# Kernel tuning notes

Hardware: AMD Instinct MI355X
Metric: run time of the kernel (lower is better)

Reference implementation:

```python
import jax, jax.numpy as jnp
import numpy as np

D_MODEL = 1024
SCALE = 1.0 / np.sqrt(D_MODEL).astype(np.float32)


def setup_inputs() -> dict:
    key = jax.random.key(0)
    ks = jax.random.split(key, 9)
    B, S, D = 4, 2048, D_MODEL
    init = 1.0 / np.sqrt(D).astype(np.float32)
    return {
        "q": jax.random.normal(ks[0], (B, S, D), jnp.float32),
        "k": jax.random.normal(ks[1], (B, S, D), jnp.float32),
        "v": jax.random.normal(ks[2], (B, S, D), jnp.float32),
        "Wq": jax.random.uniform(ks[3], (D, D), jnp.float32, -init, init),
        "bq": jax.random.uniform(ks[4], (D,), jnp.float32, -init, init),
        "Wk": jax.random.uniform(ks[5], (D, D), jnp.float32, -init, init),
        "bk": jax.random.uniform(ks[6], (D,), jnp.float32, -init, init),
        "Wv": jax.random.uniform(ks[7], (D, D), jnp.float32, -init, init),
        "bv": jax.random.uniform(ks[8], (D,), jnp.float32, -init, init),
    }


def reference(q, k, v, Wq, bq, Wk, bk, Wv, bv):
    # Linear projections (torch Linear: x @ W.T + b)
    qp = jnp.einsum('bsd,ed->bse', q, Wq) + bq
    kp = jnp.einsum('bsd,ed->bse', k, Wk) + bk
    vp = jnp.einsum('bsd,ed->bse', v, Wv) + bv
    qp = jax.nn.softmax(qp, axis=-1)          # softmax over feature dim
    kp = jax.nn.softmax(kp, axis=-2) * SCALE  # softmax over sequence dim
    vp = jax.nn.softmax(vp, axis=-2)          # softmax over sequence dim
    attn_weights = jnp.einsum('bqd,bkd->bqk', qp, kp)  # [B,S,S]
    output = jnp.einsum('bqk,bkd->bqd', attn_weights, vp)
    return (output, attn_weights)
```

## Files before the change

kernel.cpp:

```cpp
#include <hip/hip_runtime.h>
#include <math.h>


typedef float  f32x4  __attribute__((ext_vector_type(4)));
typedef __bf16 bf16x8 __attribute__((ext_vector_type(8)));
typedef int    i32x4  __attribute__((ext_vector_type(4)));
typedef unsigned short u16;

__device__ __forceinline__ float b2f(u16 u) {
    unsigned int i = ((unsigned int)u) << 16; float f;
    __builtin_memcpy(&f, &i, 4); return f;
}
__device__ __forceinline__ u16 f2b(float f) {
    unsigned int i; __builtin_memcpy(&i, &f, 4);
    i += 0x7FFFu + ((i >> 16) & 1u);
    return (u16)(i >> 16);
}

__global__ __launch_bounds__(256) void cvt_all(
    const float4* __restrict__ q, const float4* __restrict__ k,
    const float4* __restrict__ v, const float4* __restrict__ Wq,
    const float4* __restrict__ Wk, const float4* __restrict__ Wv,
    const float* __restrict__ bq, const float* __restrict__ bk,
    const float* __restrict__ bv,
    ushort4* __restrict__ qb, ushort4* __restrict__ kb,
    ushort4* __restrict__ vb, ushort4* __restrict__ Wb,
    float* __restrict__ biasCat)
{
    int bid = blockIdx.x, t = threadIdx.x;
    const float4* s; ushort4* d; int idx;
    if (bid < 8192)       { s = q;  d = qb;            idx = bid * 256 + t; }
    else if (bid < 16384) { s = k;  d = kb;            idx = (bid - 8192) * 256 + t; }
    else if (bid < 24576) { s = v;  d = vb;            idx = (bid - 16384) * 256 + t; }
    else if (bid < 25600) { s = Wq; d = Wb;            idx = (bid - 24576) * 256 + t; }
    else if (bid < 26624) { s = Wk; d = Wb + 262144;   idx = (bid - 25600) * 256 + t; }
    else if (bid < 27648) { s = Wv; d = Wb + 524288;   idx = (bid - 26624) * 256 + t; }
    else {
        for (int i = t; i < 3072; i += 256)
            biasCat[i] = (i < 1024) ? bq[i] : (i < 2048) ? bk[i - 1024] : bv[i - 2048];
        return;
    }
    float4 vv = s[idx];
    ushort4 o;
    o.x = f2b(vv.x); o.y = f2b(vv.y); o.z = f2b(vv.z); o.w = f2b(vv.w);
    d[idx] = o;
}

template<int EPI, int BN>
__global__ __launch_bounds__(512, 2) void gemm256(
    const u16* __restrict__ Ap, const u16* __restrict__ Bp,
    float* __restrict__ C32, u16* __restrict__ C16, u16* __restrict__ Calt,
    const float* __restrict__ bias,
    int N, int K, long long sA, long long sB, long long sC)
{
    constexpr int NB2 = BN / 128;
    constexpr int BH  = BN * 32;
    constexpr int LDSN = 32768 + 4 * BH;
    __shared__ __align__(16) u16 lds[LDSN];

    const int tid  = threadIdx.x;
    const int lane = tid & 63;
    const int w    = tid >> 6;
    const int wr   = w >> 2, wc = w & 3;

    const int gx  = gridDim.x;
    const int tot = gx * gridDim.y;
    const int lin = blockIdx.y * gx + blockIdx.x;
    const int vlin = (lin & 7) * (tot >> 3) + (lin >> 3);
    const int bx = vlin % gx, by = vlin / gx;
    const int m0 = by * 256, n0 = bx * BN;
    const int z  = blockIdx.z;

    const u16* Ag = Ap + (size_t)z * sA;
    const u16* Bg = Bp + (size_t)z * sB;

    const int cl = tid ^ ((tid & 32) >> 4);
    const int lr = cl >> 3;
    const int ce = (cl & 7) * 8;
    const int arow = m0 + lr;
    const int brow = (BN == 256) ? (n0 + (lr & 31) + ((lr & 32) << 1))
                                 : (n0 + lr);

    const int axr = ((lane >> 2) & 1) << 4;
    const int ar0 = (wr * 64 + (lane & 15)) * 64 + (lane >> 4) * 8;
    const int br0 = (BN == 256)
        ? ((wc * 32 + (lane & 15)) * 64 + (lane >> 4) * 8)
        : ((wc * 16 + (lane & 15)) * 64 + (lane >> 4) * 8);

#define GLL16(gsrc, ldsoff)                                                    \
    __builtin_amdgcn_global_load_lds(                                          \
        (__attribute__((address_space(1))) void*)(uintptr_t)(gsrc),            \
        (__attribute__((address_space(3))) void*)&lds[ldsoff], 16, 0, 0)

#define STAGE_A(c, h, T)                                                       \
    do { const u16* _s = Ag + (size_t)(arow + (h) * 64) * K + (T) * 64 + ce;   \
         int _d = (((c) << 1) + (h)) * 8192 + tid * 8;                         \
         GLL16(_s, _d); GLL16(_s + (size_t)128 * K, _d + 4096); } while (0)

#define STAGE_B(c, g, T)                                                       \
    do { if constexpr (BN == 256) {                                            \
             const u16* _s = Bg + (size_t)(brow + (g) * 32) * K + (T) * 64 + ce; \
             int _d = 32768 + (((c) << 1) + (g)) * 8192 + tid * 8;             \
             GLL16(_s, _d); GLL16(_s + (size_t)128 * K, _d + 4096);            \
         } else {                                                              \
             const u16* _s = Bg + (size_t)(brow + (g) * 64) * K + (T) * 64 + ce; \
             int _d = 32768 + (((c) << 1) + (g)) * 4096 + tid * 8;             \
             GLL16(_s, _d);                                                    \
         } } while (0)

#define SBAR asm volatile("s_barrier" ::: "memory")
#define LGKM0 do { asm volatile("s_waitcnt lgkmcnt(0)" ::: "memory");          \
                   __builtin_amdgcn_sched_barrier(0); } while (0)
#define VMBOUND do { if constexpr (BN == 256)                                  \
                         asm volatile("s_waitcnt vmcnt(4)" ::: "memory");      \
                     else asm volatile("s_waitcnt vmcnt(3)" ::: "memory"); } while (0)

#define LDA(base)                                                              \
    _Pragma("unroll") for (int mi2 = 0; mi2 < 4; ++mi2)                        \
    _Pragma("unroll") for (int ks = 0; ks < 2; ++ks)                           \
        afr[mi2][ks] = __builtin_bit_cast(bf16x8,                              \
            *(const i32x4*)&lds[(base) + ((ar0 + mi2 * 1024 + ks * 32) ^ axr)]);

#define LDB(dst, base)                                                         \
    _Pragma("unroll") for (int ni2 = 0; ni2 < NB2; ++ni2)                      \
    _Pragma("unroll") for (int ks = 0; ks < 2; ++ks)                           \
        dst[ni2][ks] = __builtin_bit_cast(bf16x8,                              \
            *(const i32x4*)&lds[(base) + ((br0 + ni2 * 1024 + ks * 32) ^ axr)]);

#define MFMA_Q(mb, nb, bfrag)                                                  \
    __builtin_amdgcn_s_setprio(1);                                             \
    _Pragma("unroll") for (int mi2 = 0; mi2 < 4; ++mi2)                        \
    _Pragma("unroll") for (int ni2 = 0; ni2 < NB2; ++ni2)                      \
    _Pragma("unroll") for (int ks = 0; ks < 2; ++ks)                           \
        acc[(mb) + mi2][(nb) + ni2] = __builtin_amdgcn_mfma_f32_16x16x32_bf16( \
            afr[mi2][ks], bfrag[ni2][ks], acc[(mb) + mi2][(nb) + ni2], 0, 0, 0); \
    __builtin_amdgcn_s_setprio(0)

    f32x4 acc[8][2 * NB2];
#pragma unroll
    for (int i = 0; i < 8; ++i)
#pragma unroll
        for (int j = 0; j < 2 * NB2; ++j) acc[i][j] = (f32x4)0.0f;

    bf16x8 afr[4][2], b0f[NB2][2], b1f[NB2][2];

    const int nt = K >> 6;

    STAGE_A(0, 0, 0); STAGE_B(0, 0, 0);
    STAGE_A(0, 1, 0); STAGE_B(0, 1, 0);
    STAGE_A(1, 0, 1); STAGE_B(1, 0, 1);

    for (int T = 0; T < nt; ++T) {
        const int cur = T & 1, nxt = cur ^ 1;
        const int ab = (cur << 1) * 8192;
        const int bb = 32768 + (cur << 1) * BH;

        if (T + 1 < nt) VMBOUND;
        else            asm volatile("s_waitcnt vmcnt(0)" ::: "memory");
        SBAR;
        LDA(ab); LDB(b0f, bb);
        if (T + 1 < nt) STAGE_B(nxt, 1, T + 1);
        SBAR; LGKM0;
        MFMA_Q(0, 0, b0f);
        SBAR;
        LDB(b1f, bb + BH);
        if (T + 1 < nt) STAGE_A(nxt, 1, T + 1);
        SBAR; LGKM0;
        MFMA_Q(0, NB2, b1f);
        SBAR;
        LDA(ab + 8192);
        if (T + 2 < nt) STAGE_A(cur, 0, T + 2);
        SBAR; LGKM0;
        MFMA_Q(4, 0, b0f);
        SBAR;
        if (T + 2 < nt) STAGE_B(cur, 0, T + 2);
        SBAR; LGKM0;
        MFMA_Q(4, NB2, b1f);
        SBAR;
    }

    const int cr0 = m0 + wr * 128 + ((lane >> 4) << 2);

    if constexpr (EPI == 0) {
        const int cc0 = n0 + wc * 64 + (lane & 15);
        float* Cg = C32 + (size_t)z * sC;
#pragma unroll
        for (int mi = 0; mi < 8; ++mi)
#pragma unroll
            for (int ni = 0; ni < 4; ++ni)
#pragma unroll
                for (int j = 0; j < 4; ++j)
                    Cg[(size_t)(cr0 + mi * 16 + j) * N + cc0 + ni * 16] = acc[mi][ni][j];

        u16* sE = lds;
        u16* Cb = C16 + (size_t)z * sC;
        const int wrow0 = ((lane >> 4) << 2);
        const int wcol0 = wc * 64 + (lane & 15);
        const int rr = tid >> 2;
        const int c0 = (tid & 3) * 8;
        __syncthreads();
#pragma unroll
        for (int p = 0; p < 2; ++p) {
            if (wr == p) {
#pragma unroll
                for (int mi = 0; mi < 8; ++mi)
#pragma unroll
                    for (int ni = 0; ni < 4; ++ni)
#pragma unroll
                        for (int j = 0; j < 4; ++j)
                            sE[(wrow0 + mi * 16 + j) * 264 + wcol0 + ni * 16] =
                                f2b(acc[mi][ni][j]);
            }
            __syncthreads();
#pragma unroll
            for (int i = 0; i < 8; ++i) {
                i32x4 vv = *(const i32x4*)&sE[rr * 264 + c0 + i * 32];
                *(i32x4*)&Cb[(size_t)(m0 + p * 128 + rr) * N + n0 + c0 + i * 32] = vv;
            }
            if (p == 0) __syncthreads();
        }
    } else if constexpr (EPI == 1) {
        u16* sE = lds;
        u16* Cb = (z == 2) ? Calt : (C16 + (size_t)z * sC);
        const int colb = wc * 16 + (lane & 15);
        const float bv0 = bias[(size_t)z * 1024 + n0 + colb];
        const float bv1 = bias[(size_t)z * 1024 + n0 + 64 + colb];
        const int wrow0 = ((lane >> 4) << 2);
        const int rr = tid >> 2, t4 = tid & 3;
        __syncthreads();
#pragma unroll
        for (int p = 0; p < 2; ++p) {
            if (wr == p) {
#pragma unroll
                for (int mi = 0; mi < 8; ++mi)
#pragma unroll
                    for (int j = 0; j < 4; ++j) {
                        int row = wrow0 + mi * 16 + j;
                        sE[row * 136 + colb]      = f2b(__expf(acc[mi][0][j] + bv0));
                        sE[row * 136 + 64 + colb] = f2b(__expf(acc[mi][1][j] + bv1));
                    }
            }
            __syncthreads();
#pragma unroll
            for (int i = 0; i < 4; ++i) {
                i32x4 vv = *(const i32x4*)&sE[rr * 136 + (t4 + i * 4) * 8];
                *(i32x4*)&Cb[(size_t)(m0 + p * 128 + rr) * N + n0 + (t4 + i * 4) * 8] = vv;
            }
            if (p == 0) __syncthreads();
        }
    } else {
        float* Cg = C32 + (size_t)z * sC;
        const int colb = wc * 16 + (lane & 15);
#pragma unroll
        for (int mi = 0; mi < 8; ++mi)
#pragma unroll
            for (int ni = 0; ni < 2; ++ni)
#pragma unroll
                for (int j = 0; j < 4; ++j)
                    Cg[(size_t)(cr0 + mi * 16 + j) * N + n0 + ni * 64 + colb] =
                        acc[mi][ni][j];
    }
#undef GLL16
#undef STAGE_A
#undef STAGE_B
#undef SBAR
#undef LGKM0
#undef VMBOUND
#undef LDA
#undef LDB
#undef MFMA_Q
}

__global__ __launch_bounds__(256) void sm_partials(
    u16* __restrict__ qE, const u16* __restrict__ kE, const u16* __restrict__ vE,
    float* __restrict__ kpart, float* __restrict__ vpart)
{
    int bid = blockIdx.x, t = threadIdx.x;
    if (bid < 8192) {
        u16* p = qE + (size_t)bid * 1024;
        ushort4 v = *(ushort4*)&p[t * 4];
        float e0 = b2f(v.x), e1 = b2f(v.y), e2 = b2f(v.z), e3 = b2f(v.w);
        float s = (e0 + e1) + (e2 + e3);
#pragma unroll
        for (int off = 32; off; off >>= 1) s += __shfl_down(s, off);
        __shared__ float red[4];
        if ((t & 63) == 0) red[t >> 6] = s;
        __syncthreads();
        float inv = 1.0f / ((red[0] + red[1]) + (red[2] + red[3]));
        ushort4 o;
        o.x = f2b(e0 * inv); o.y = f2b(e1 * inv);
        o.z = f2b(e2 * inv); o.w = f2b(e3 * inv);
        *(ushort4*)&p[t * 4] = o;
    } else {
        int j = bid - 8192;
        const u16* d; float* part;
        if (j < 64) { d = kE; part = kpart; } else { d = vE; part = vpart; j -= 64; }
        int b = j >> 4, c = j & 15;
        const u16* base = d + ((size_t)b * 2048 + c * 128) * 1024 + t * 4;
        float a0 = 0, a1 = 0, a2 = 0, a3 = 0;
        for (int s = 0; s < 128; ++s) {
            ushort4 v = *(const ushort4*)(base + (size_t)s * 1024);
            a0 += b2f(v.x); a1 += b2f(v.y); a2 += b2f(v.z); a3 += b2f(v.w);
        }
        *(float4*)(part + ((size_t)(b * 16 + c)) * 1024 + t * 4) = make_float4(a0, a1, a2, a3);
    }
}

__global__ __launch_bounds__(256) void col_reduce2(
    const float* __restrict__ kpart, const float* __restrict__ vpart,
    float* __restrict__ kinv, float* __restrict__ vinv)
{
    int bid = blockIdx.x;
    const float* part; float* inv; float mult;
    if (bid < 16) { part = kpart; inv = kinv; mult = 0.03125f; }
    else          { part = vpart; inv = vinv; mult = 1.0f; bid -= 16; }
    int idx = bid * 256 + threadIdx.x;
    int b = idx >> 10, e = idx & 1023;
    float s = 0;
    for (int c = 0; c < 16; ++c) s += part[((size_t)(b * 16 + c)) * 1024 + e];
    inv[idx] = mult / s;
}

__global__ __launch_bounds__(256) void norm_all(
    u16* __restrict__ kE, const float* __restrict__ kinv,
    const u16* __restrict__ vE, const float* __restrict__ vinv,
    u16* __restrict__ vpT)
{
    int bid = blockIdx.x, t = threadIdx.x;
    if (bid < 8192) {
        int b = bid >> 11, s = bid & 2047;
        u16* p = kE + ((size_t)b * 2048 + s) * 1024 + t * 4;
        float4 iv = *(const float4*)(kinv + b * 1024 + t * 4);
        ushort4 v = *(ushort4*)p;
        v.x = f2b(b2f(v.x) * iv.x); v.y = f2b(b2f(v.y) * iv.y);
        v.z = f2b(b2f(v.z) * iv.z); v.w = f2b(b2f(v.w) * iv.w);
        *(ushort4*)p = v;
    } else {
        __shared__ __align__(16) u16 tile[64][68];
        int j = bid - 8192;
        int b = j >> 9, y = (j >> 5) & 15, x = j & 31;
        int s0 = x * 64, e0 = y * 64;
        int lr = t >> 4, lc = (t & 15) * 4;
#pragma unroll
        for (int i = 0; i < 4; ++i) {
            int sr = i * 16 + lr;
            ushort4 v = *(const ushort4*)(vE + ((size_t)b * 2048 + s0 + sr) * 1024 + e0 + lc);
            tile[sr][lc] = v.x; tile[sr][lc + 1] = v.y;
            tile[sr][lc + 2] = v.z; tile[sr][lc + 3] = v.w;
        }
        __syncthreads();
#pragma unroll
        for (int i = 0; i < 4; ++i) {
            int er = i * 16 + lr;
            float iv = vinv[b * 1024 + e0 + er];
            ushort4 v;
            v.x = f2b(b2f(tile[lc + 0][er]) * iv);
            v.y = f2b(b2f(tile[lc + 1][er]) * iv);
            v.z = f2b(b2f(tile[lc + 2][er]) * iv);
            v.w = f2b(b2f(tile[lc + 3][er]) * iv);
            *(ushort4*)(vpT + ((size_t)b * 1024 + e0 + er) * 2048 + s0 + lc) = v;
        }
    }
}

extern "C" void kernel_launch(void* const* d_in, const int* in_sizes, int n_in,
                              void* d_out, int out_size, void* d_ws, size_t ws_size,
                              hipStream_t stream)
{
    const float* q  = (const float*)d_in[0];
    const float* k  = (const float*)d_in[1];
    const float* v  = (const float*)d_in[2];
    const float* Wq = (const float*)d_in[3];
    const float* bq = (const float*)d_in[4];
    const float* Wk = (const float*)d_in[5];
    const float* bk = (const float*)d_in[6];
    const float* Wv = (const float*)d_in[7];
    const float* bv = (const float*)d_in[8];

    float* out  = (float*)d_out;
    float* attn = out + 8388608;

    u16* wsU = (u16*)d_ws;
    u16* qE   = wsU;
    u16* kE   = wsU + 8388608;
    u16* Wb   = wsU + 16777216;
    u16* qb   = wsU + 25165824;
    u16* kb   = wsU + 33554432;
    u16* vb   = wsU + 41943040;
    u16* vpT  = wsU + 25165824;
    u16* attnB = wsU + 33554432;
    u16* vE   = (u16*)attn;

    float* tail  = (float*)(wsU + 50331648);
    float* kpart = tail;
    float* vpart = tail + 65536;
    float* kinv  = tail + 131072;
    float* vinv  = tail + 135168;
    float* biasCat = tail + 139264;

    const long long SD = 2048LL * 1024, SS = 2048LL * 2048, DS = 1024LL * 2048;

    cvt_all<<<dim3(27649), dim3(256), 0, stream>>>(
        (const float4*)q, (const float4*)k, (const float4*)v,
        (const float4*)Wq, (const float4*)Wk, (const float4*)Wv,
        bq, bk, bv,
        (ushort4*)qb, (ushort4*)kb, (ushort4*)vb, (ushort4*)Wb, biasCat);

    gemm256<1, 128><<<dim3(8, 32, 3), dim3(512), 0, stream>>>(
        qb, Wb, nullptr, qE, vE, biasCat,
        1024, 1024, 8388608LL, 1048576LL, 8388608LL);

    sm_partials<<<dim3(8320), dim3(256), 0, stream>>>(qE, kE, vE, kpart, vpart);

    col_reduce2<<<dim3(32), dim3(256), 0, stream>>>(kpart, vpart, kinv, vinv);

    norm_all<<<dim3(10240), dim3(256), 0, stream>>>(kE, kinv, vE, vinv, vpT);

    gemm256<0, 256><<<dim3(8, 8, 4), dim3(512), 0, stream>>>(
        qE, kE, attn, attnB, nullptr, nullptr, 2048, 1024, SD, SD, SS);

    gemm256<2, 128><<<dim3(8, 8, 4), dim3(512), 0, stream>>>(
        attnB, vpT, out, nullptr, nullptr, nullptr, 1024, 2048, SS, DS, SD);
}
```

Measured before the change: 245.4 us.

## Restructure BN=128 GEMM pipeline to two barrier phases and swizzle epilogue LDS

For the BN=128 GEMM variant, the K loop is rebuilt into two phases per tile. Both B fragments are loaded at once and staging is regrouped, which cuts the number of s_barrier/lgkmcnt waits per iteration from eight to two, with retuned vmcnt thresholds. The BN=256 path is kept but inlined. Both epilogues now XOR-swizzle LDS column addresses by row to reduce bank conflicts when staging bf16 output. Fewer barriers per tile risk read/write hazards on the LDS buffers if the vmcnt accounting is off.

```diff
diff --git a/kernel.cpp b/kernel.cpp
--- a/kernel.cpp
+++ b/kernel.cpp
@@ -111,9 +111,6 @@
 #define SBAR asm volatile("s_barrier" ::: "memory")
 #define LGKM0 do { asm volatile("s_waitcnt lgkmcnt(0)" ::: "memory");          \
                    __builtin_amdgcn_sched_barrier(0); } while (0)
-#define VMBOUND do { if constexpr (BN == 256)                                  \
-                         asm volatile("s_waitcnt vmcnt(4)" ::: "memory");      \
-                     else asm volatile("s_waitcnt vmcnt(3)" ::: "memory"); } while (0)
 
 #define LDA(base)                                                              \
     _Pragma("unroll") for (int mi2 = 0; mi2 < 4; ++mi2)                        \
@@ -146,37 +143,66 @@
 
     const int nt = K >> 6;
 
-    STAGE_A(0, 0, 0); STAGE_B(0, 0, 0);
-    STAGE_A(0, 1, 0); STAGE_B(0, 1, 0);
-    STAGE_A(1, 0, 1); STAGE_B(1, 0, 1);
-
-    for (int T = 0; T < nt; ++T) {
-        const int cur = T & 1, nxt = cur ^ 1;
-        const int ab = (cur << 1) * 8192;
-        const int bb = 32768 + (cur << 1) * BH;
-
-        if (T + 1 < nt) VMBOUND;
-        else            asm volatile("s_waitcnt vmcnt(0)" ::: "memory");
-        SBAR;
-        LDA(ab); LDB(b0f, bb);
-        if (T + 1 < nt) STAGE_B(nxt, 1, T + 1);
-        SBAR; LGKM0;
-        MFMA_Q(0, 0, b0f);
-        SBAR;
-        LDB(b1f, bb + BH);
-        if (T + 1 < nt) STAGE_A(nxt, 1, T + 1);
-        SBAR; LGKM0;
-        MFMA_Q(0, NB2, b1f);
-        SBAR;
-        LDA(ab + 8192);
-        if (T + 2 < nt) STAGE_A(cur, 0, T + 2);
-        SBAR; LGKM0;
-        MFMA_Q(4, 0, b0f);
-        SBAR;
-        if (T + 2 < nt) STAGE_B(cur, 0, T + 2);
-        SBAR; LGKM0;
-        MFMA_Q(4, NB2, b1f);
-        SBAR;
+    if constexpr (BN == 256) {
+        STAGE_A(0, 0, 0); STAGE_B(0, 0, 0);
+        STAGE_A(0, 1, 0); STAGE_B(0, 1, 0);
+        STAGE_A(1, 0, 1); STAGE_B(1, 0, 1);
+
+        for (int T = 0; T < nt; ++T) {
+            const int cur = T & 1, nxt = cur ^ 1;
+            const int ab = (cur << 1) * 8192;
+            const int bb = 32768 + (cur << 1) * BH;
+
+            if (T + 1 < nt) asm volatile("s_waitcnt vmcnt(4)" ::: "memory");
+            else            asm volatile("s_waitcnt vmcnt(0)" ::: "memory");
+            SBAR;
+            LDA(ab); LDB(b0f, bb);
+            if (T + 1 < nt) STAGE_B(nxt, 1, T + 1);
+            SBAR; LGKM0;
+            MFMA_Q(0, 0, b0f);
+            SBAR;
+            LDB(b1f, bb + BH);
+            if (T + 1 < nt) STAGE_A(nxt, 1, T + 1);
+            SBAR; LGKM0;
+            MFMA_Q(0, NB2, b1f);
+            SBAR;
+            LDA(ab + 8192);
+            if (T + 2 < nt) STAGE_A(cur, 0, T + 2);
+            SBAR; LGKM0;
+            MFMA_Q(4, 0, b0f);
+            SBAR;
+            if (T + 2 < nt) STAGE_B(cur, 0, T + 2);
+            SBAR; LGKM0;
+            MFMA_Q(4, NB2, b1f);
+            SBAR;
+        }
+    } else {
+        STAGE_A(0, 0, 0); STAGE_B(0, 0, 0); STAGE_B(0, 1, 0);
+        STAGE_A(0, 1, 0);
+        STAGE_A(1, 0, 1); STAGE_B(1, 0, 1); STAGE_B(1, 1, 1);
+
+        for (int T = 0; T < nt; ++T) {
+            const int cur = T & 1, nxt = cur ^ 1;
+            const int ab = (cur << 1) * 8192;
+            const int bb = 32768 + (cur << 1) * BH;
+
+            if (T + 1 < nt) asm volatile("s_waitcnt vmcnt(6)" ::: "memory");
+            else            asm volatile("s_waitcnt vmcnt(2)" ::: "memory");
+            SBAR;
+            LDA(ab); LDB(b0f, bb); LDB(b1f, bb + BH);
+            if (T + 1 < nt) STAGE_A(nxt, 1, T + 1);
+            LGKM0;
+            MFMA_Q(0, 0, b0f); MFMA_Q(0, 1, b1f);
+
+            if (T + 1 < nt) asm volatile("s_waitcnt vmcnt(6)" ::: "memory");
+            else            asm volatile("s_waitcnt vmcnt(0)" ::: "memory");
+            SBAR;
+            LDA(ab + 8192);
+            if (T + 2 < nt) { STAGE_A(cur, 0, T + 2); STAGE_B(cur, 0, T + 2);
+                              STAGE_B(cur, 1, T + 2); }
+            LGKM0;
+            MFMA_Q(4, 0, b0f); MFMA_Q(4, 1, b1f);
+        }
     }
 
     const int cr0 = m0 + wr * 128 + ((lane >> 4) << 2);
@@ -198,6 +224,7 @@
         const int wcol0 = wc * 64 + (lane & 15);
         const int rr = tid >> 2;
         const int c0 = (tid & 3) * 8;
+        const int rxor = ((rr >> 2) & 3) << 4;
         __syncthreads();
 #pragma unroll
         for (int p = 0; p < 2; ++p) {
@@ -205,16 +232,19 @@
 #pragma unroll
                 for (int mi = 0; mi < 8; ++mi)
 #pragma unroll
-                    for (int ni = 0; ni < 4; ++ni)
-#pragma unroll
-                        for (int j = 0; j < 4; ++j)
-                            sE[(wrow0 + mi * 16 + j) * 264 + wcol0 + ni * 16] =
+                    for (int j = 0; j < 4; ++j) {
+                        int row = wrow0 + mi * 16 + j;
+                        int cx = ((row >> 2) & 3) << 4;
+#pragma unroll
+                        for (int ni = 0; ni < 4; ++ni)
+                            sE[row * 264 + ((wcol0 + ni * 16) ^ cx)] =
                                 f2b(acc[mi][ni][j]);
+                    }
             }
             __syncthreads();
 #pragma unroll
             for (int i = 0; i < 8; ++i) {
-                i32x4 vv = *(const i32x4*)&sE[rr * 264 + c0 + i * 32];
+                i32x4 vv = *(const i32x4*)&sE[rr * 264 + ((c0 + i * 32) ^ rxor)];
                 *(i32x4*)&Cb[(size_t)(m0 + p * 128 + rr) * N + n0 + c0 + i * 32] = vv;
             }
             if (p == 0) __syncthreads();
@@ -227,6 +257,7 @@
         const float bv1 = bias[(size_t)z * 1024 + n0 + 64 + colb];
         const int wrow0 = ((lane >> 4) << 2);
         const int rr = tid >> 2, t4 = tid & 3;
+        const int rxor = ((rr >> 2) & 3) << 4;
         __syncthreads();
 #pragma unroll
         for (int p = 0; p < 2; ++p) {
@@ -236,14 +267,15 @@
 #pragma unroll
                     for (int j = 0; j < 4; ++j) {
                         int row = wrow0 + mi * 16 + j;
-                        sE[row * 136 + colb]      = f2b(__expf(acc[mi][0][j] + bv0));
-                        sE[row * 136 + 64 + colb] = f2b(__expf(acc[mi][1][j] + bv1));
+                        int cx = ((row >> 2) & 3) << 4;
+                        sE[row * 136 + (colb ^ cx)]        = f2b(__expf(acc[mi][0][j] + bv0));
+                        sE[row * 136 + ((64 + colb) ^ cx)] = f2b(__expf(acc[mi][1][j] + bv1));
                     }
             }
             __syncthreads();
 #pragma unroll
             for (int i = 0; i < 4; ++i) {
-                i32x4 vv = *(const i32x4*)&sE[rr * 136 + (t4 + i * 4) * 8];
+                i32x4 vv = *(const i32x4*)&sE[rr * 136 + (((t4 + i * 4) * 8) ^ rxor)];
                 *(i32x4*)&Cb[(size_t)(m0 + p * 128 + rr) * N + n0 + (t4 + i * 4) * 8] = vv;
             }
             if (p == 0) __syncthreads();
@@ -265,7 +297,6 @@
 #undef STAGE_B
 #undef SBAR
 #undef LGKM0
-#undef VMBOUND
 #undef LDA
 #undef LDB
 #undef MFMA_Q
```

Result: faster. 224.0 us (-8.7%).

## Use 128x128 tile GEMM for projections and output, widen LDS swizzle for attn GEMM

Applied to the files above, without the earlier changes.

Adds a new 128x128-tile GEMM kernel with 4 blocks per CU and a simpler two-phase K pipeline. It is used for the QKV projection and the attn@V GEMM, which doubles or quadruples their grid sizes to improve occupancy and CU load balance. The 256x256 QK^T kernel becomes a specialised non-template kernel with a wider XOR swizzle meant to cut LDS bank conflicts. Smaller tiles mean less data reuse per block and more global traffic.

```diff
diff --git a/kernel.cpp b/kernel.cpp
--- a/kernel.cpp
+++ b/kernel.cpp
@@ -46,17 +46,12 @@
     d[idx] = o;
 }
 
-template<int EPI, int BN>
-__global__ __launch_bounds__(512, 2) void gemm256(
+__global__ __launch_bounds__(512, 2) void gemm256_attn(
     const u16* __restrict__ Ap, const u16* __restrict__ Bp,
-    float* __restrict__ C32, u16* __restrict__ C16, u16* __restrict__ Calt,
-    const float* __restrict__ bias,
+    float* __restrict__ C32, u16* __restrict__ C16,
     int N, int K, long long sA, long long sB, long long sC)
 {
-    constexpr int NB2 = BN / 128;
-    constexpr int BH  = BN * 32;
-    constexpr int LDSN = 32768 + 4 * BH;
-    __shared__ __align__(16) u16 lds[LDSN];
+    __shared__ __align__(16) u16 lds[65536];
 
     const int tid  = threadIdx.x;
     const int lane = tid & 63;
@@ -68,24 +63,21 @@
     const int lin = blockIdx.y * gx + blockIdx.x;
     const int vlin = (lin & 7) * (tot >> 3) + (lin >> 3);
     const int bx = vlin % gx, by = vlin / gx;
-    const int m0 = by * 256, n0 = bx * BN;
+    const int m0 = by * 256, n0 = bx * 256;
     const int z  = blockIdx.z;
 
     const u16* Ag = Ap + (size_t)z * sA;
     const u16* Bg = Bp + (size_t)z * sB;
 
-    const int cl = tid ^ ((tid & 32) >> 4);
+    const int cl = tid ^ ((tid >> 4) & 6);
     const int lr = cl >> 3;
     const int ce = (cl & 7) * 8;
     const int arow = m0 + lr;
-    const int brow = (BN == 256) ? (n0 + (lr & 31) + ((lr & 32) << 1))
-                                 : (n0 + lr);
-
-    const int axr = ((lane >> 2) & 1) << 4;
+    const int brow = n0 + (lr & 31) + ((lr & 32) << 1);
+
+    const int axr = ((lane >> 2) & 3) << 4;
     const int ar0 = (wr * 64 + (lane & 15)) * 64 + (lane >> 4) * 8;
-    const int br0 = (BN == 256)
-        ? ((wc * 32 + (lane & 15)) * 64 + (lane >> 4) * 8)
-        : ((wc * 16 + (lane & 15)) * 64 + (lane >> 4) * 8);
+    const int br0 = (wc * 32 + (lane & 15)) * 64 + (lane >> 4) * 8;
 
 #define GLL16(gsrc, ldsoff)                                                    \
     __builtin_amdgcn_global_load_lds(                                          \
@@ -98,22 +90,13 @@
          GLL16(_s, _d); GLL16(_s + (size_t)128 * K, _d + 4096); } while (0)
 
 #define STAGE_B(c, g, T)                                                       \
-    do { if constexpr (BN == 256) {                                            \
-             const u16* _s = Bg + (size_t)(brow + (g) * 32) * K + (T) * 64 + ce; \
-             int _d = 32768 + (((c) << 1) + (g)) * 8192 + tid * 8;             \
-             GLL16(_s, _d); GLL16(_s + (size_t)128 * K, _d + 4096);            \
-         } else {                                                              \
-             const u16* _s = Bg + (size_t)(brow + (g) * 64) * K + (T) * 64 + ce; \
-             int _d = 32768 + (((c) << 1) + (g)) * 4096 + tid * 8;             \
-             GLL16(_s, _d);                                                    \
-         } } while (0)
+    do { const u16* _s = Bg + (size_t)(brow + (g) * 32) * K + (T) * 64 + ce;   \
+         int _d = 32768 + (((c) << 1) + (g)) * 8192 + tid * 8;                 \
+         GLL16(_s, _d); GLL16(_s + (size_t)128 * K, _d + 4096); } while (0)
 
 #define SBAR asm volatile("s_barrier" ::: "memory")
 #define LGKM0 do { asm volatile("s_waitcnt lgkmcnt(0)" ::: "memory");          \
                    __builtin_amdgcn_sched_barrier(0); } while (0)
-#define VMBOUND do { if constexpr (BN == 256)                                  \
-                         asm volatile("s_waitcnt vmcnt(4)" ::: "memory");      \
-                     else asm volatile("s_waitcnt vmcnt(3)" ::: "memory"); } while (0)
 
 #define LDA(base)                                                              \
     _Pragma("unroll") for (int mi2 = 0; mi2 < 4; ++mi2)                        \
@@ -122,7 +105,7 @@
             *(const i32x4*)&lds[(base) + ((ar0 + mi2 * 1024 + ks * 32) ^ axr)]);
 
 #define LDB(dst, base)                                                         \
-    _Pragma("unroll") for (int ni2 = 0; ni2 < NB2; ++ni2)                      \
+    _Pragma("unroll") for (int ni2 = 0; ni2 < 2; ++ni2)                        \
     _Pragma("unroll") for (int ks = 0; ks < 2; ++ks)                           \
         dst[ni2][ks] = __builtin_bit_cast(bf16x8,                              \
             *(const i32x4*)&lds[(base) + ((br0 + ni2 * 1024 + ks * 32) ^ axr)]);
@@ -130,19 +113,19 @@
 #define MFMA_Q(mb, nb, bfrag)                                                  \
     __builtin_amdgcn_s_setprio(1);                                             \
     _Pragma("unroll") for (int mi2 = 0; mi2 < 4; ++mi2)                        \
-    _Pragma("unroll") for (int ni2 = 0; ni2 < NB2; ++ni2)                      \
+    _Pragma("unroll") for (int ni2 = 0; ni2 < 2; ++ni2)                        \
     _Pragma("unroll") for (int ks = 0; ks < 2; ++ks)                           \
         acc[(mb) + mi2][(nb) + ni2] = __builtin_amdgcn_mfma_f32_16x16x32_bf16( \
             afr[mi2][ks], bfrag[ni2][ks], acc[(mb) + mi2][(nb) + ni2], 0, 0, 0); \
     __builtin_amdgcn_s_setprio(0)
 
-    f32x4 acc[8][2 * NB2];
+    f32x4 acc[8][4];
 #pragma unroll
     for (int i = 0; i < 8; ++i)
 #pragma unroll
-        for (int j = 0; j < 2 * NB2; ++j) acc[i][j] = (f32x4)0.0f;
-
-    bf16x8 afr[4][2], b0f[NB2][2], b1f[NB2][2];
+        for (int j = 0; j < 4; ++j) acc[i][j] = (f32x4)0.0f;
+
+    bf16x8 afr[4][2], b0f[2][2], b1f[2][2];
 
     const int nt = K >> 6;
 
@@ -153,9 +136,9 @@
     for (int T = 0; T < nt; ++T) {
         const int cur = T & 1, nxt = cur ^ 1;
         const int ab = (cur << 1) * 8192;
-        const int bb = 32768 + (cur << 1) * BH;
-
-        if (T + 1 < nt) VMBOUND;
+        const int bb = 32768 + (cur << 1) * 8192;
+
+        if (T + 1 < nt) asm volatile("s_waitcnt vmcnt(4)" ::: "memory");
         else            asm volatile("s_waitcnt vmcnt(0)" ::: "memory");
         SBAR;
         LDA(ab); LDB(b0f, bb);
@@ -163,10 +146,10 @@
         SBAR; LGKM0;
         MFMA_Q(0, 0, b0f);
         SBAR;
-        LDB(b1f, bb + BH);
+        LDB(b1f, bb + 8192);
         if (T + 1 < nt) STAGE_A(nxt, 1, T + 1);
         SBAR; LGKM0;
-        MFMA_Q(0, NB2, b1f);
+        MFMA_Q(0, 2, b1f);
         SBAR;
         LDA(ab + 8192);
         if (T + 2 < nt) STAGE_A(cur, 0, T + 2);
@@ -175,100 +158,199 @@
         SBAR;
         if (T + 2 < nt) STAGE_B(cur, 0, T + 2);
         SBAR; LGKM0;
-        MFMA_Q(4, NB2, b1f);
+        MFMA_Q(4, 2, b1f);
         SBAR;
     }
 
     const int cr0 = m0 + wr * 128 + ((lane >> 4) << 2);
-
-    if constexpr (EPI == 0) {
-        const int cc0 = n0 + wc * 64 + (lane & 15);
-        float* Cg = C32 + (size_t)z * sC;
-#pragma unroll
-        for (int mi = 0; mi < 8; ++mi)
-#pragma unroll
-            for (int ni = 0; ni < 4; ++ni)
-#pragma unroll
-                for (int j = 0; j < 4; ++j)
-                    Cg[(size_t)(cr0 + mi * 16 + j) * N + cc0 + ni * 16] = acc[mi][ni][j];
-
-        u16* sE = lds;
-        u16* Cb = C16 + (size_t)z * sC;
-        const int wrow0 = ((lane >> 4) << 2);
-        const int wcol0 = wc * 64 + (lane & 15);
-        const int rr = tid >> 2;
-        const int c0 = (tid & 3) * 8;
+    const int cc0 = n0 + wc * 64 + (lane & 15);
+    float* Cg = C32 + (size_t)z * sC;
+#pragma unroll
+    for (int mi = 0; mi < 8; ++mi)
+#pragma unroll
+        for (int ni = 0; ni < 4; ++ni)
+#pragma unroll
+            for (int j = 0; j < 4; ++j)
+                Cg[(size_t)(cr0 + mi * 16 + j) * N + cc0 + ni * 16] = acc[mi][ni][j];
+
+    u16* sE = lds;
+    u16* Cb = C16 + (size_t)z * sC;
+    const int wrow0 = ((lane >> 4) << 2);
+    const int wcol0 = wc * 64 + (lane & 15);
+    const int rr = tid >> 2;
+    const int c0 = (tid & 3) * 8;
+    __syncthreads();
+#pragma unroll
+    for (int p = 0; p < 2; ++p) {
+        if (wr == p) {
+#pragma unroll
+            for (int mi = 0; mi < 8; ++mi)
+#pragma unroll
+                for (int ni = 0; ni < 4; ++ni)
+#pragma unroll
+                    for (int j = 0; j < 4; ++j)
+                        sE[(wrow0 + mi * 16 + j) * 264 + wcol0 + ni * 16] =
+                            f2b(acc[mi][ni][j]);
+        }
         __syncthreads();
 #pragma unroll
-        for (int p = 0; p < 2; ++p) {
-            if (wr == p) {
-#pragma unroll
-                for (int mi = 0; mi < 8; ++mi)
-#pragma unroll
-                    for (int ni = 0; ni < 4; ++ni)
-#pragma unroll
-                        for (int j = 0; j < 4; ++j)
-                            sE[(wrow0 + mi * 16 + j) * 264 + wcol0 + ni * 16] =
-                                f2b(acc[mi][ni][j]);
-            }
-            __syncthreads();
-#pragma unroll
-            for (int i = 0; i < 8; ++i) {
-                i32x4 vv = *(const i32x4*)&sE[rr * 264 + c0 + i * 32];
-                *(i32x4*)&Cb[(size_t)(m0 + p * 128 + rr) * N + n0 + c0 + i * 32] = vv;
-            }
-            if (p == 0) __syncthreads();
+        for (int i = 0; i < 8; ++i) {
+            i32x4 vv = *(const i32x4*)&sE[rr * 264 + c0 + i * 32];
+            *(i32x4*)&Cb[(size_t)(m0 + p * 128 + rr) * N + n0 + c0 + i * 32] = vv;
         }
-    } else if constexpr (EPI == 1) {
+        if (p == 0) __syncthreads();
+    }
+#undef GLL16
+#undef STAGE_A
+#undef STAGE_B
+#undef LDA
+#undef LDB
+#undef MFMA_Q
+}
+
+template<int EPI>
+__global__ __launch_bounds__(512, 4) void gemm128(
+    const u16* __restrict__ Ap, const u16* __restrict__ Bp,
+    float* __restrict__ C32, u16* __restrict__ C16, u16* __restrict__ Calt,
+    const float* __restrict__ bias,
+    int N, int K, long long sA, long long sB, long long sC)
+{
+    __shared__ __align__(16) u16 lds[32768];
+
+    const int tid  = threadIdx.x;
+    const int lane = tid & 63;
+    const int w    = tid >> 6;
+    const int wr   = w >> 2, wc = w & 3;
+
+    const int gx  = gridDim.x;
+    const int tot = gx * gridDim.y;
+    const int lin = blockIdx.y * gx + blockIdx.x;
+    const int vlin = (lin & 7) * (tot >> 3) + (lin >> 3);
+    const int bx = vlin % gx, by = vlin / gx;
+    const int m0 = by * 128, n0 = bx * 128;
+    const int z  = blockIdx.z;
+
+    const u16* Ag = Ap + (size_t)z * sA;
+    const u16* Bg = Bp + (size_t)z * sB;
+
+    const int cl = tid ^ ((tid >> 3) & 3);
+    const int lr = cl >> 2;
+    const int ce = (cl & 3) * 8;
+    const int arow = m0 + lr, brow = n0 + lr;
+
+    const int exr = ((lane >> 1) & 3) << 3;
+    const int ar0 = (wr * 64 + (lane & 15)) * 32 + (lane >> 4) * 8;
+    const int br0 = (wc * 32 + (lane & 15)) * 32 + (lane >> 4) * 8;
+
+#define GLL16(gsrc, ldsoff)                                                    \
+    __builtin_amdgcn_global_load_lds(                                          \
+        (__attribute__((address_space(1))) void*)(uintptr_t)(gsrc),            \
+        (__attribute__((address_space(3))) void*)&lds[ldsoff], 16, 0, 0)
+
+#define STAGE_A(c, h, T)                                                       \
+    GLL16(Ag + (size_t)arow * K + (T) * 64 + (h) * 32 + ce,                    \
+          (((c) << 1) + (h)) * 4096 + tid * 8)
+
+#define STAGE_B(c, h, T)                                                       \
+    GLL16(Bg + (size_t)brow * K + (T) * 64 + (h) * 32 + ce,                    \
+          16384 + (((c) << 1) + (h)) * 4096 + tid * 8)
+
+#define LGKM0 do { asm volatile("s_waitcnt lgkmcnt(0)" ::: "memory");          \
+                   __builtin_amdgcn_sched_barrier(0); } while (0)
+
+#define LDAB(base)                                                             \
+    _Pragma("unroll") for (int mi2 = 0; mi2 < 4; ++mi2)                        \
+        afr[mi2] = __builtin_bit_cast(bf16x8,                                  \
+            *(const i32x4*)&lds[(base) + ((ar0 + mi2 * 512) ^ exr)]);          \
+    _Pragma("unroll") for (int ni2 = 0; ni2 < 2; ++ni2)                        \
+        bfr[ni2] = __builtin_bit_cast(bf16x8,                                  \
+            *(const i32x4*)&lds[16384 + (base) + ((br0 + ni2 * 512) ^ exr)]);
+
+#define MFMA8                                                                  \
+    __builtin_amdgcn_s_setprio(1);                                             \
+    _Pragma("unroll") for (int mi2 = 0; mi2 < 4; ++mi2)                        \
+    _Pragma("unroll") for (int ni2 = 0; ni2 < 2; ++ni2)                        \
+        acc[mi2][ni2] = __builtin_amdgcn_mfma_f32_16x16x32_bf16(               \
+            afr[mi2], bfr[ni2], acc[mi2][ni2], 0, 0, 0);                       \
+    __builtin_amdgcn_s_setprio(0)
+
+    f32x4 acc[4][2];
+#pragma unroll
+    for (int i = 0; i < 4; ++i)
+#pragma unroll
+        for (int j = 0; j < 2; ++j) acc[i][j] = (f32x4)0.0f;
+
+    bf16x8 afr[4], bfr[2];
+
+    const int nt = K >> 6;
+
+    STAGE_A(0, 0, 0); STAGE_B(0, 0, 0);
+    STAGE_A(0, 1, 0); STAGE_B(0, 1, 0);
+    STAGE_A(1, 0, 1); STAGE_B(1, 0, 1);
+
+    for (int T = 0; T < nt; ++T) {
+        const int cur = T & 1, nxt = cur ^ 1;
+        const int ab = (cur << 1) * 4096;
+
+        if (T + 1 < nt) asm volatile("s_waitcnt vmcnt(4)" ::: "memory");
+        else            asm volatile("s_waitcnt vmcnt(2)" ::: "memory");
+        asm volatile("s_barrier" ::: "memory");
+        LDAB(ab);
+        if (T + 1 < nt) { STAGE_A(nxt, 1, T + 1); STAGE_B(nxt, 1, T + 1); }
+        LGKM0;
+        MFMA8;
+
+        if (T + 1 < nt) asm volatile("s_waitcnt vmcnt(4)" ::: "memory");
+        else            asm volatile("s_waitcnt vmcnt(0)" ::: "memory");
+        asm volatile("s_barrier" ::: "memory");
+        LDAB(ab + 4096);
+        if (T + 2 < nt) { STAGE_A(cur, 0, T + 2); STAGE_B(cur, 0, T + 2); }
+        LGKM0;
+        MFMA8;
+    }
+
+    if constexpr (EPI == 1) {
         u16* sE = lds;
         u16* Cb = (z == 2) ? Calt : (C16 + (size_t)z * sC);
-        const int colb = wc * 16 + (lane & 15);
-        const float bv0 = bias[(size_t)z * 1024 + n0 + colb];
-        const float bv1 = bias[(size_t)z * 1024 + n0 + 64 + colb];
-        const int wrow0 = ((lane >> 4) << 2);
-        const int rr = tid >> 2, t4 = tid & 3;
+        const int colb = wc * 32 + (lane & 15);
+        float bv0 = bias[(size_t)z * 1024 + n0 + colb];
+        float bv1 = bias[(size_t)z * 1024 + n0 + colb + 16];
+        const int wrow0 = wr * 64 + ((lane >> 4) << 2);
         __syncthreads();
 #pragma unroll
-        for (int p = 0; p < 2; ++p) {
-            if (wr == p) {
-#pragma unroll
-                for (int mi = 0; mi < 8; ++mi)
-#pragma unroll
-                    for (int j = 0; j < 4; ++j) {
-                        int row = wrow0 + mi * 16 + j;
-                        sE[row * 136 + colb]      = f2b(__expf(acc[mi][0][j] + bv0));
-                        sE[row * 136 + 64 + colb] = f2b(__expf(acc[mi][1][j] + bv1));
-                    }
+        for (int mi = 0; mi < 4; ++mi)
+#pragma unroll
+            for (int j = 0; j < 4; ++j) {
+                int row = wrow0 + mi * 16 + j;
+                sE[row * 136 + colb]      = f2b(__expf(acc[mi][0][j] + bv0));
+                sE[row * 136 + colb + 16] = f2b(__expf(acc[mi][1][j] + bv1));
             }
-            __syncthreads();
-#pragma unroll
-            for (int i = 0; i < 4; ++i) {
-                i32x4 vv = *(const i32x4*)&sE[rr * 136 + (t4 + i * 4) * 8];
-                *(i32x4*)&Cb[(size_t)(m0 + p * 128 + rr) * N + n0 + (t4 + i * 4) * 8] = vv;
-            }
-            if (p == 0) __syncthreads();
+        __syncthreads();
+        const int rr = tid >> 2, c0 = (tid & 3) * 8;
+#pragma unroll
+        for (int i = 0; i < 4; ++i) {
+            i32x4 vv = *(const i32x4*)&sE[rr * 136 + c0 + i * 32];
+            *(i32x4*)&Cb[(size_t)(m0 + rr) * N + n0 + c0 + i * 32] = vv;
         }
     } else {
         float* Cg = C32 + (size_t)z * sC;
-        const int colb = wc * 16 + (lane & 15);
-#pragma unroll
-        for (int mi = 0; mi < 8; ++mi)
+        const int cr0 = m0 + wr * 64 + ((lane >> 4) << 2);
+        const int cc0 = n0 + wc * 32 + (lane & 15);
+#pragma unroll
+        for (int mi = 0; mi < 4; ++mi)
 #pragma unroll
             for (int ni = 0; ni < 2; ++ni)
 #pragma unroll
                 for (int j = 0; j < 4; ++j)
-                    Cg[(size_t)(cr0 + mi * 16 + j) * N + n0 + ni * 64 + colb] =
+                    Cg[(size_t)(cr0 + mi * 16 + j) * N + cc0 + ni * 16] =
                         acc[mi][ni][j];
     }
 #undef GLL16
 #undef STAGE_A
 #undef STAGE_B
-#undef SBAR
 #undef LGKM0
-#undef VMBOUND
-#undef LDA
-#undef LDB
-#undef MFMA_Q
+#undef LDAB
+#undef MFMA8
 }
 
 __global__ __launch_bounds__(256) void sm_partials(
@@ -406,7 +488,7 @@
         bq, bk, bv,
         (ushort4*)qb, (ushort4*)kb, (ushort4*)vb, (ushort4*)Wb, biasCat);
 
-    gemm256<1, 128><<<dim3(8, 32, 3), dim3(512), 0, stream>>>(
+    gemm128<1><<<dim3(8, 64, 3), dim3(512), 0, stream>>>(
         qb, Wb, nullptr, qE, vE, biasCat,
         1024, 1024, 8388608LL, 1048576LL, 8388608LL);
 
@@ -416,9 +498,9 @@
 
     norm_all<<<dim3(10240), dim3(256), 0, stream>>>(kE, kinv, vE, vinv, vpT);
 
-    gemm256<0, 256><<<dim3(8, 8, 4), dim3(512), 0, stream>>>(
-        qE, kE, attn, attnB, nullptr, nullptr, 2048, 1024, SD, SD, SS);
-
-    gemm256<2, 128><<<dim3(8, 8, 4), dim3(512), 0, stream>>>(
+    gemm256_attn<<<dim3(8, 8, 4), dim3(512), 0, stream>>>(
+        qE, kE, attn, attnB, 2048, 1024, SD, SD, SS);
+
+    gemm128<2><<<dim3(8, 16, 4), dim3(512), 0, stream>>>(
         attnB, vpT, out, nullptr, nullptr, nullptr, 1024, 2048, SS, DS, SD);
 }
```

After: 221.4 us. 9.8% less time.
